# Optimization experiments

Hardware: AMD Instinct MI355X
Metric: run time of the kernel (lower is better)

Reference implementation:

```python
import jax, jax.numpy as jnp
import numpy as np


def build_mask_even(kh, kw):
    # Hexnet build_masks: zero one edge column for kernel rows at odd distance
    # from the kernel center (hex neighborhood); returns even-row mask + shift.
    mask = np.ones((kh, kw), dtype=np.float32)
    center = kh // 2
    shift = -1 if center % 2 else 1
    for r in range(kh):
        if abs(center - r) % 2:
            if shift == 1:
                mask[r, -1] = 0.0
            else:
                mask[r, 0] = 0.0
    return mask, shift


def setup_inputs() -> dict:
    key = jax.random.key(0)
    k1, k2, k3 = jax.random.split(key, 3)
    x = jax.random.normal(k1, (16, 128, 128, 128), dtype=jnp.float32)  # NHWC
    kernel = jax.random.normal(k2, (3, 3, 128, 256), dtype=jnp.float32) * 0.05  # HWIO
    bias = jax.random.normal(k3, (256,), dtype=jnp.float32) * 0.05
    return {"x": x, "kernel": kernel, "bias": bias}


def _hconv(x, kernel, bias):
    kh, kw = kernel.shape[0], kernel.shape[1]
    mask_np, shift = build_mask_even(kh, kw)
    kernel_even = kernel * jnp.asarray(mask_np)[:, :, None, None]

    # Odd-row kernel: only the rows at odd distance from center, rolled along width.
    center = kh // 2
    odd_rows = [jnp.roll(kernel_even[r], shift, axis=0)
                for r in range(kh) if abs(center - r) % 2]
    kernel_odd = jnp.stack(odd_rows, axis=0)  # (n_odd, kw, Cin, F)

    dn = ("NHWC", "HWIO", "NHWC")
    strides = (2, 1)  # build() doubles the H stride
    out_even = jax.lax.conv_general_dilated(
        x, kernel_even, window_strides=strides, padding="SAME",
        dimension_numbers=dn)
    out_odd = jax.lax.conv_general_dilated(
        x[:, 1:], kernel_odd, window_strides=strides, padding="SAME",
        dimension_numbers=dn)

    # Interleave rows: even0, odd0, even1, odd1, ... (+ trailing even row if longer)
    he, ho = out_even.shape[1], out_odd.shape[1]
    hm = min(he, ho)
    b, _, w, f = out_even.shape
    out = jnp.stack([out_even[:, :hm], out_odd[:, :hm]], axis=2)
    out = out.reshape(b, 2 * hm, w, f)
    if he > ho:
        out = jnp.concatenate([out, out_even[:, -1:]], axis=1)

    return jax.nn.relu(out + bias)


def reference(x, kernel, bias):
    return _hconv(x, kernel, bias)
```

## Files before the change

kernel.cpp:

```cpp
#include <hip/hip_runtime.h>


#define N_  16
#define H_  128
#define W_  128
#define C_  128
#define F_  256
#define HP  130
#define WP  130

typedef short bf16x8 __attribute__((ext_vector_type(8)));
typedef float f32x4  __attribute__((ext_vector_type(4)));

__device__ __forceinline__ unsigned int bf_bits(float f) {
  unsigned int u = __float_as_uint(f);
  return (u + 0x7FFFu + ((u >> 16) & 1u)) >> 16;
}
__device__ __forceinline__ unsigned int pack2(float a, float b) {
  return bf_bits(a) | (bf_bits(b) << 16);
}

__device__ __forceinline__ void even_tap(int ti, int& dr, int& dc, int& kr, int& kc) {
  switch (ti) {
    case 0:  dr = 0; dc = 0;  kr = 0; kc = 1; break;
    case 1:  dr = 0; dc = 1;  kr = 0; kc = 2; break;
    case 2:  dr = 1; dc = -1; kr = 1; kc = 0; break;
    case 3:  dr = 1; dc = 0;  kr = 1; kc = 1; break;
    case 4:  dr = 1; dc = 1;  kr = 1; kc = 2; break;
    case 5:  dr = 2; dc = 0;  kr = 2; kc = 1; break;
    default: dr = 2; dc = 1;  kr = 2; kc = 2; break;
  }
}

__global__ __launch_bounds__(256) void prep_xpad(
    const float* __restrict__ x, char* __restrict__ xpad) {
  long id = (long)blockIdx.x * 256 + threadIdx.x;
  const long total = (long)N_ * HP * WP * 16;
  if (id >= total) return;
  const int g  = (int)(id & 7);
  const int hc = (int)((id >> 3) & 1);
  long pix = id >> 4;
  const int wp = (int)(pix % WP);
  long t = pix / WP;
  const int hh = (int)(t % HP);
  const int nn = (int)(t / HP);
  const int ww = wp - 1;
  const int key = ww & 7;
  uint4 o = make_uint4(0u, 0u, 0u, 0u);
  if (hh < H_ && ww >= 0 && ww < W_) {
    const float* s = x + (((long)(nn * H_ + hh) * W_ + ww) * C_ + hc * 64 + (g ^ key) * 8);
    float4 a = *(const float4*)s;
    float4 b = *(const float4*)(s + 4);
    o.x = pack2(a.x, a.y); o.y = pack2(a.z, a.w);
    o.z = pack2(b.x, b.y); o.w = pack2(b.z, b.w);
  }
  *(uint4*)(xpad + id * 16) = o;
}

__global__ __launch_bounds__(256) void prep_wt2(
    const float* __restrict__ k, char* __restrict__ wt2) {
  int id = blockIdx.x * 256 + threadIdx.x;
  if (id >= 7 * 2 * 2 * 128 * 8) return;
  const int g  = id & 7;
  const int f  = (id >> 3) & 127;
  const int ft = (id >> 10) & 1;
  const int hc = (id >> 11) & 1;
  const int ti = id >> 12;
  int dr, dc, kr, kc;
  even_tap(ti, dr, dc, kr, kc);
  const int fg = ft * 128 + f;
  const int c0 = hc * 64 + (g ^ (f & 7)) * 8;
  float v[8];
#pragma unroll
  for (int j = 0; j < 8; ++j)
    v[j] = k[((size_t)(kr * 3 + kc) * C_ + (c0 + j)) * F_ + fg];
  uint4 o;
  o.x = pack2(v[0], v[1]); o.y = pack2(v[2], v[3]);
  o.z = pack2(v[4], v[5]); o.w = pack2(v[6], v[7]);
  *(uint4*)(wt2 + (size_t)id * 16) = o;
}

__global__ __launch_bounds__(256, 3) void hconv_mfma(
    const char* __restrict__ xpad,
    const char* __restrict__ wt2,
    const float* __restrict__ bias,
    float* __restrict__ out) {
  __shared__ __align__(16) char smem[32768];

  const int tid = threadIdx.x;
  const int bid = (blockIdx.x & 7) * 512 + (blockIdx.x >> 3);
  const int ft = bid & 1;
  const int h  = (bid >> 1) & 127;
  const int n  = bid >> 8;
  const int p  = h & 1;
  const int nsteps = p ? 8 : 14;

  const int lane = tid & 63;
  const int wid  = tid >> 6;
  const int wr   = wid >> 1;
  const int wc   = wid & 1;
  const int l16  = lane & 15;
  const int lk   = lane >> 4;

  auto step_info = [&](int s, int& dc, int& widx, int& dr) {
    if (p == 0) {
      int ti = s >> 1; widx = ti;
      int kr, kc; even_tap(ti, dr, dc, kr, kc);
    } else {
      int q = s >> 1;
      dr = q >> 1;
      dc = (q & 1) ? 0 : -1;
      widx = (q == 0) ? 0 : (q == 1) ? 1 : (q == 2) ? 5 : 6;
    }
  };

  auto stage = [&](int s) {
    int dc, widx, dr; step_info(s, dc, widx, dr);
    const int hc = s & 1;
    const long rowbase = (long)(n * HP + (h + dr)) * WP;
#pragma unroll
    for (int i = 0; i < 4; ++i) {
      const int L = i * 256 + tid;
      const int row = L >> 3, slot = L & 7;
      const char* src = xpad + (rowbase + (row + dc + 1)) * 256 + hc * 128 + slot * 16;
      __builtin_amdgcn_global_load_lds(
          (const __attribute__((address_space(1))) void*)src,
          (__attribute__((address_space(3))) void*)(smem + L * 16), 16, 0, 0);
    }
    const char* bsrc = wt2 + (size_t)((widx * 2 + hc) * 2 + ft) * 16384;
#pragma unroll
    for (int i = 0; i < 4; ++i) {
      const int L = i * 256 + tid;
      __builtin_amdgcn_global_load_lds(
          (const __attribute__((address_space(1))) void*)(bsrc + L * 16),
          (__attribute__((address_space(3))) void*)(smem + 16384 + L * 16), 16, 0, 0);
    }
  };

  f32x4 acc[4][4] = {};

  stage(0);
  __syncthreads();

  for (int s = 0; s < nsteps; ++s) {
    int dc, widx, dr; step_info(s, dc, widx, dr);
    const char* ab = (const char*)smem;
    const char* bb = (const char*)smem + 16384;

    bf16x8 af[4][2], bfr[4][2];
#pragma unroll
    for (int m = 0; m < 4; ++m) {
      const int wl  = wr * 64 + m * 16 + l16;
      const int key = (wl + dc) & 7;
#pragma unroll
      for (int kk = 0; kk < 2; ++kk)
        af[m][kk] = *(const bf16x8*)(ab + wl * 128 + (((kk * 4 + lk) ^ key) * 16));
    }
#pragma unroll
    for (int fi = 0; fi < 4; ++fi) {
      const int fl = wc * 64 + fi * 16 + l16;
#pragma unroll
      for (int kk = 0; kk < 2; ++kk)
        bfr[fi][kk] = *(const bf16x8*)(bb + fl * 128 + (((kk * 4 + lk) ^ (fl & 7)) * 16));
    }

#pragma unroll
    for (int m = 0; m < 4; ++m)
#pragma unroll
      for (int fi = 0; fi < 4; ++fi)
#pragma unroll
        for (int kk = 0; kk < 2; ++kk)
          acc[m][fi] = __builtin_amdgcn_mfma_f32_16x16x32_bf16(
              af[m][kk], bfr[fi][kk], acc[m][fi], 0, 0, 0);

    __syncthreads();
    if (s + 1 < nsteps) stage(s + 1);
    __syncthreads();
  }

#pragma unroll
  for (int fi = 0; fi < 4; ++fi) {
    const int f = ft * 128 + wc * 64 + fi * 16 + l16;
    const float bv = bias[f];
#pragma unroll
    for (int m = 0; m < 4; ++m) {
      const int w = wr * 64 + m * 16 + lk * 4;
      float* o = out + (((size_t)(n * H_ + h) * W_ + w) * F_ + f);
#pragma unroll
      for (int r = 0; r < 4; ++r) {
        float v = acc[m][fi][r] + bv;
        v = v > 0.f ? v : 0.f;
        o[(size_t)r * F_] = v;
      }
    }
  }
}

__device__ __forceinline__ void tap_info11(int t, int& dr, int& dc, int& kr, int& kc) {
  switch (t) {
    case 0:  dr = 0; dc = 0;  kr = 0; kc = 1; break;
    case 1:  dr = 0; dc = 1;  kr = 0; kc = 2; break;
    case 2:  dr = 1; dc = -1; kr = 1; kc = 0; break;
    case 3:  dr = 1; dc = 0;  kr = 1; kc = 1; break;
    case 4:  dr = 1; dc = 1;  kr = 1; kc = 2; break;
    case 5:  dr = 2; dc = 0;  kr = 2; kc = 1; break;
    case 6:  dr = 2; dc = 1;  kr = 2; kc = 2; break;
    case 7:  dr = 0; dc = -1; kr = 0; kc = 1; break;
    case 8:  dr = 0; dc = 0;  kr = 0; kc = 2; break;
    case 9:  dr = 1; dc = -1; kr = 2; kc = 1; break;
    default: dr = 1; dc = 0;  kr = 2; kc = 2; break;
  }
}

__global__ __launch_bounds__(256) void build_w_fb(
    const float* __restrict__ k, unsigned short* __restrict__ wt) {
  int tid = blockIdx.x * 256 + threadIdx.x;
  if (tid >= 11 * F_ * C_) return;
  int c = tid & 127;
  int f = (tid >> 7) & 255;
  int t = tid >> 15;
  int dr, dc, kr, kc;
  tap_info11(t, dr, dc, kr, kc);
  wt[tid] = (unsigned short)bf_bits(k[((kr * 3 + kc) * C_ + c) * F_ + f]);
}

__global__ __launch_bounds__(256, 3) void hconv_fb(
    const float* __restrict__ x,
    const unsigned short* __restrict__ wt,
    const float* __restrict__ bias,
    float* __restrict__ out) {
  __shared__ __align__(16) char smem[49152];
  const int tid = threadIdx.x;
  const int bid = (blockIdx.x & 7) * 1024 + (blockIdx.x >> 3);
  const int ft    = bid & 1;
  const int wtile = (bid >> 1) & 1;
  const int h     = (bid >> 2) & 127;
  const int n     = bid >> 9;
  const int f0 = ft * 128;
  const int w0 = wtile * 64;
  const int p  = h & 1;
  const int tap0   = p ? 7 : 0;
  const int nsteps = p ? 8 : 14;
  const int lane = tid & 63;
  const int wid  = tid >> 6;
  const int l16  = lane & 15;
  const int lk   = lane >> 4;
  const int awl = tid >> 2;
  const int ag2 = tid & 3;
  const int bfl   = tid >> 1;
  const int bhalf = tid & 1;
  float4 ar0, ar1, ar2, ar3;
  uint4  br0, br1, br2, br3;
  auto load_step = [&](int s) {
    const int tap = tap0 + (s >> 1);
    const int cc  = s & 1;
    int dr, dc, kr, kc;
    tap_info11(tap, dr, dc, kr, kc);
    const int hh = h + dr;
    const int wg = w0 + awl + dc;
    const bool av = (hh < H_) && (wg >= 0) && (wg < W_);
    if (av) {
      const float* ap = x + (((long)(n * H_ + hh) * W_ + wg) * C_ + cc * 64 + ag2 * 16);
      ar0 = *(const float4*)(ap);
      ar1 = *(const float4*)(ap + 4);
      ar2 = *(const float4*)(ap + 8);
      ar3 = *(const float4*)(ap + 12);
    } else {
      ar0 = ar1 = ar2 = ar3 = make_float4(0.f, 0.f, 0.f, 0.f);
    }
    const unsigned short* bp =
        wt + ((size_t)(tap * F_ + f0 + bfl) * C_ + cc * 64 + bhalf * 32);
    const uint4* bq = (const uint4*)bp;
    br0 = bq[0]; br1 = bq[1]; br2 = bq[2]; br3 = bq[3];
  };
  auto write_step = [&](int sel) {
    uint4 u0, u1;
    u0.x = pack2(ar0.x, ar0.y); u0.y = pack2(ar0.z, ar0.w);
    u0.z = pack2(ar1.x, ar1.y); u0.w = pack2(ar1.z, ar1.w);
    u1.x = pack2(ar2.x, ar2.y); u1.y = pack2(ar2.z, ar2.w);
    u1.z = pack2(ar3.x, ar3.y); u1.w = pack2(ar3.z, ar3.w);
    char* abase = (char*)smem + sel * 8192 + awl * 128;
    const int sw = awl & 7;
    *(uint4*)(abase + (((2 * ag2)     ^ sw) * 16)) = u0;
    *(uint4*)(abase + (((2 * ag2 + 1) ^ sw) * 16)) = u1;
    char* bbase = (char*)smem + 16384 + sel * 16384 + bfl * 128;
    const int sb = bfl & 7;
    *(uint4*)(bbase + (((bhalf * 4 + 0) ^ sb) * 16)) = br0;
    *(uint4*)(bbase + (((bhalf * 4 + 1) ^ sb) * 16)) = br1;
    *(uint4*)(bbase + (((bhalf * 4 + 2) ^ sb) * 16)) = br2;
    *(uint4*)(bbase + (((bhalf * 4 + 3) ^ sb) * 16)) = br3;
  };
  f32x4 acc[4][2] = {};
  load_step(0);
  write_step(0);
  load_step(1);
  __syncthreads();
  for (int s = 0; s < nsteps; ++s) {
    const int cur = s & 1;
    const char* ab = (const char*)smem + cur * 8192;
    const char* bb = (const char*)smem + 16384 + cur * 16384;
    bf16x8 af[4][2], bfr[2][2];
#pragma unroll
    for (int m = 0; m < 4; ++m)
#pragma unroll
      for (int kkk = 0; kkk < 2; ++kkk) {
        const int wl = m * 16 + l16;
        const int g  = (kkk * 4 + lk) ^ (wl & 7);
        af[m][kkk] = *(const bf16x8*)(ab + wl * 128 + g * 16);
      }
#pragma unroll
    for (int fi = 0; fi < 2; ++fi)
#pragma unroll
      for (int kkk = 0; kkk < 2; ++kkk) {
        const int fl = wid * 32 + fi * 16 + l16;
        const int g  = (kkk * 4 + lk) ^ (fl & 7);
        bfr[fi][kkk] = *(const bf16x8*)(bb + fl * 128 + g * 16);
      }
    if (s + 1 < nsteps) write_step(cur ^ 1);
    if (s + 2 < nsteps) load_step(s + 2);
#pragma unroll
    for (int m = 0; m < 4; ++m)
#pragma unroll
      for (int fi = 0; fi < 2; ++fi)
#pragma unroll
        for (int kkk = 0; kkk < 2; ++kkk)
          acc[m][fi] = __builtin_amdgcn_mfma_f32_16x16x32_bf16(
              af[m][kkk], bfr[fi][kkk], acc[m][fi], 0, 0, 0);
    __syncthreads();
  }
#pragma unroll
  for (int fi = 0; fi < 2; ++fi) {
    const int f = f0 + wid * 32 + fi * 16 + l16;
    const float bv = bias[f];
#pragma unroll
    for (int m = 0; m < 4; ++m) {
      const int w = w0 + m * 16 + lk * 4;
      float* o = out + (((size_t)(n * H_ + h) * W_ + w) * F_ + f);
#pragma unroll
      for (int r = 0; r < 4; ++r) {
        float v = acc[m][fi][r] + bv;
        v = v > 0.f ? v : 0.f;
        o[(size_t)r * F_] = v;
      }
    }
  }
}

extern "C" void kernel_launch(void* const* d_in, const int* in_sizes, int n_in,
                              void* d_out, int out_size, void* d_ws, size_t ws_size,
                              hipStream_t stream) {
  const float* x    = (const float*)d_in[0];
  const float* kern = (const float*)d_in[1];
  const float* bias = (const float*)d_in[2];
  float* out = (float*)d_out;

  const size_t XPAD_BYTES = (size_t)N_ * HP * WP * 256;
  const size_t WT2_BYTES  = (size_t)7 * 2 * 2 * 128 * 8 * 16;

  if (ws_size >= XPAD_BYTES + WT2_BYTES) {
    char* xpad = (char*)d_ws;
    char* wt2  = (char*)d_ws + XPAD_BYTES;
    {
      const long total = (long)N_ * HP * WP * 16;
      prep_xpad<<<(int)((total + 255) / 256), 256, 0, stream>>>(x, xpad);
    }
    prep_wt2<<<112, 256, 0, stream>>>(kern, wt2);
    hconv_mfma<<<N_ * H_ * 2, 256, 0, stream>>>(xpad, wt2, bias, out);
  } else {
    unsigned short* wt = (unsigned short*)d_ws;
    build_w_fb<<<(11 * F_ * C_ + 255) / 256, 256, 0, stream>>>(kern, wt);
    hconv_fb<<<N_ * H_ * 2 * 2, 256, 0, stream>>>(x, wt, bias, out);
  }
}
```

Measured before the change: 172.0 us.

## Load activation fragments directly from a channel-group-major padded layout, double-buffer weights

```diff
diff --git a/kernel.cpp b/kernel.cpp
--- a/kernel.cpp
+++ b/kernel.cpp
@@ -32,29 +32,25 @@
   }
 }
 
-__global__ __launch_bounds__(256) void prep_xpad(
-    const float* __restrict__ x, char* __restrict__ xpad) {
+__global__ __launch_bounds__(256) void prep_xpad2(
+    const float* __restrict__ x, char* __restrict__ xp) {
   long id = (long)blockIdx.x * 256 + threadIdx.x;
-  const long total = (long)N_ * HP * WP * 16;
-  if (id >= total) return;
-  const int g  = (int)(id & 7);
-  const int hc = (int)((id >> 3) & 1);
-  long pix = id >> 4;
-  const int wp = (int)(pix % WP);
-  long t = pix / WP;
+  const int wp = (int)(id % WP);
+  long t = id / WP;
+  const int g  = (int)(t & 15);
+  t >>= 4;
   const int hh = (int)(t % HP);
   const int nn = (int)(t / HP);
   const int ww = wp - 1;
-  const int key = ww & 7;
   uint4 o = make_uint4(0u, 0u, 0u, 0u);
   if (hh < H_ && ww >= 0 && ww < W_) {
-    const float* s = x + (((long)(nn * H_ + hh) * W_ + ww) * C_ + hc * 64 + (g ^ key) * 8);
+    const float* s = x + (((long)(nn * H_ + hh) * W_ + ww) * C_ + g * 8);
     float4 a = *(const float4*)s;
     float4 b = *(const float4*)(s + 4);
     o.x = pack2(a.x, a.y); o.y = pack2(a.z, a.w);
     o.z = pack2(b.x, b.y); o.w = pack2(b.z, b.w);
   }
-  *(uint4*)(xpad + id * 16) = o;
+  *(uint4*)(xp + id * 16) = o;
 }
 
 __global__ __launch_bounds__(256) void prep_wt2(
@@ -81,7 +77,7 @@
 }
 
 __global__ __launch_bounds__(256, 3) void hconv_mfma(
-    const char* __restrict__ xpad,
+    const char* __restrict__ xpad2,
     const char* __restrict__ wt2,
     const float* __restrict__ bias,
     float* __restrict__ out) {
@@ -114,48 +110,45 @@
     }
   };
 
-  auto stage = [&](int s) {
+  auto stageB = [&](int s, int sel) {
     int dc, widx, dr; step_info(s, dc, widx, dr);
     const int hc = s & 1;
-    const long rowbase = (long)(n * HP + (h + dr)) * WP;
-#pragma unroll
-    for (int i = 0; i < 4; ++i) {
-      const int L = i * 256 + tid;
-      const int row = L >> 3, slot = L & 7;
-      const char* src = xpad + (rowbase + (row + dc + 1)) * 256 + hc * 128 + slot * 16;
-      __builtin_amdgcn_global_load_lds(
-          (const __attribute__((address_space(1))) void*)src,
-          (__attribute__((address_space(3))) void*)(smem + L * 16), 16, 0, 0);
-    }
     const char* bsrc = wt2 + (size_t)((widx * 2 + hc) * 2 + ft) * 16384;
+    char* base = (char*)smem + sel * 16384;
 #pragma unroll
     for (int i = 0; i < 4; ++i) {
       const int L = i * 256 + tid;
       __builtin_amdgcn_global_load_lds(
           (const __attribute__((address_space(1))) void*)(bsrc + L * 16),
-          (__attribute__((address_space(3))) void*)(smem + 16384 + L * 16), 16, 0, 0);
-    }
+          (__attribute__((address_space(3))) void*)(base + L * 16), 16, 0, 0);
+    }
+  };
+
+  bf16x8 af[4][2];
+  auto issueA = [&](int s) {
+    int dc, widx, dr; step_info(s, dc, widx, dr);
+    const int hc = s & 1;
+    const char* abase = xpad2 +
+        ((long)((n * HP + (h + dr)) * 16 + hc * 8 + lk) * WP + wr * 64 + dc + 1 + l16) * 16;
+#pragma unroll
+    for (int m = 0; m < 4; ++m)
+#pragma unroll
+      for (int kk = 0; kk < 2; ++kk)
+        af[m][kk] = *(const bf16x8*)(abase + ((long)kk * 4 * WP + m * 16) * 16);
   };
 
   f32x4 acc[4][4] = {};
 
-  stage(0);
+  stageB(0, 0);
+  issueA(0);
   __syncthreads();
 
   for (int s = 0; s < nsteps; ++s) {
-    int dc, widx, dr; step_info(s, dc, widx, dr);
-    const char* ab = (const char*)smem;
-    const char* bb = (const char*)smem + 16384;
-
-    bf16x8 af[4][2], bfr[4][2];
-#pragma unroll
-    for (int m = 0; m < 4; ++m) {
-      const int wl  = wr * 64 + m * 16 + l16;
-      const int key = (wl + dc) & 7;
-#pragma unroll
-      for (int kk = 0; kk < 2; ++kk)
-        af[m][kk] = *(const bf16x8*)(ab + wl * 128 + (((kk * 4 + lk) ^ key) * 16));
-    }
+    const int cur = s & 1;
+    if (s + 1 < nsteps) stageB(s + 1, cur ^ 1);
+
+    const char* bb = (const char*)smem + cur * 16384;
+    bf16x8 bfr[4][2];
 #pragma unroll
     for (int fi = 0; fi < 4; ++fi) {
       const int fl = wc * 64 + fi * 16 + l16;
@@ -173,9 +166,10 @@
           acc[m][fi] = __builtin_amdgcn_mfma_f32_16x16x32_bf16(
               af[m][kk], bfr[fi][kk], acc[m][fi], 0, 0, 0);
 
-    __syncthreads();
-    if (s + 1 < nsteps) stage(s + 1);
-    __syncthreads();
+    if (s + 1 < nsteps) {
+      issueA(s + 1);
+      __syncthreads();
+    }
   }
 
 #pragma unroll
@@ -229,7 +223,7 @@
     const unsigned short* __restrict__ wt,
     const float* __restrict__ bias,
     float* __restrict__ out) {
-  __shared__ __align__(16) char smem[49152];
+  __shared__ __align__(16) char smem_s[49152];
   const int tid = threadIdx.x;
   const int bid = (blockIdx.x & 7) * 1024 + (blockIdx.x >> 3);
   const int ft    = bid & 1;
@@ -279,11 +273,11 @@
     u0.z = pack2(ar1.x, ar1.y); u0.w = pack2(ar1.z, ar1.w);
     u1.x = pack2(ar2.x, ar2.y); u1.y = pack2(ar2.z, ar2.w);
     u1.z = pack2(ar3.x, ar3.y); u1.w = pack2(ar3.z, ar3.w);
-    char* abase = (char*)smem + sel * 8192 + awl * 128;
+    char* abase = (char*)smem_s + sel * 8192 + awl * 128;
     const int sw = awl & 7;
     *(uint4*)(abase + (((2 * ag2)     ^ sw) * 16)) = u0;
     *(uint4*)(abase + (((2 * ag2 + 1) ^ sw) * 16)) = u1;
-    char* bbase = (char*)smem + 16384 + sel * 16384 + bfl * 128;
+    char* bbase = (char*)smem_s + 16384 + sel * 16384 + bfl * 128;
     const int sb = bfl & 7;
     *(uint4*)(bbase + (((bhalf * 4 + 0) ^ sb) * 16)) = br0;
     *(uint4*)(bbase + (((bhalf * 4 + 1) ^ sb) * 16)) = br1;
@@ -297,8 +291,8 @@
   __syncthreads();
   for (int s = 0; s < nsteps; ++s) {
     const int cur = s & 1;
-    const char* ab = (const char*)smem + cur * 8192;
-    const char* bb = (const char*)smem + 16384 + cur * 16384;
+    const char* ab = (const char*)smem_s + cur * 8192;
+    const char* bb = (const char*)smem_s + 16384 + cur * 16384;
     bf16x8 af[4][2], bfr[2][2];
 #pragma unroll
     for (int m = 0; m < 4; ++m)
@@ -354,18 +348,15 @@
   const float* bias = (const float*)d_in[2];
   float* out = (float*)d_out;
 
-  const size_t XPAD_BYTES = (size_t)N_ * HP * WP * 256;
+  const size_t XPAD_BYTES = (size_t)N_ * HP * 16 * WP * 16;
   const size_t WT2_BYTES  = (size_t)7 * 2 * 2 * 128 * 8 * 16;
 
   if (ws_size >= XPAD_BYTES + WT2_BYTES) {
-    char* xpad = (char*)d_ws;
-    char* wt2  = (char*)d_ws + XPAD_BYTES;
-    {
-      const long total = (long)N_ * HP * WP * 16;
-      prep_xpad<<<(int)((total + 255) / 256), 256, 0, stream>>>(x, xpad);
-    }
+    char* xpad2 = (char*)d_ws;
+    char* wt2   = (char*)d_ws + XPAD_BYTES;
+    prep_xpad2<<<16900, 256, 0, stream>>>(x, xpad2);
     prep_wt2<<<112, 256, 0, stream>>>(kern, wt2);
-    hconv_mfma<<<N_ * H_ * 2, 256, 0, stream>>>(xpad, wt2, bias, out);
+    hconv_mfma<<<N_ * H_ * 2, 256, 0, stream>>>(xpad2, wt2, bias, out);
   } else {
     unsigned short* wt = (unsigned short*)d_ws;
     build_w_fb<<<(11 * F_ * C_ + 255) / 256, 256, 0, stream>>>(kern, wt);
```

Result: slower. 194.4 us (+13.1%).
